# Kernel tuning notes

Hardware: AMD Instinct MI355X
Metric: run time of the kernel (lower is better)

Reference implementation:

```python
import jax, jax.numpy as jnp
import numpy as np

EMBED_DIM = 1024
NUM_HEADS = 16
HEAD_DIM = EMBED_DIM // NUM_HEADS
STD = 0.02


def setup_inputs() -> dict:
    key = jax.random.key(0)
    k1, k2, k3 = jax.random.split(key, 3)
    B, S = 2, 2048
    inputs = jax.random.normal(k1, (B, S, EMBED_DIM), dtype=jnp.float32)
    # qkv projection: Linear(E, 3E); torch Linear weight is [out, in]
    w_qkv = jax.random.normal(k2, (3 * EMBED_DIM, EMBED_DIM), dtype=jnp.float32) * STD
    b_qkv = jnp.zeros((3 * EMBED_DIM,), dtype=jnp.float32)
    w_out = jax.random.normal(k3, (EMBED_DIM, EMBED_DIM), dtype=jnp.float32) * STD
    b_out = jnp.zeros((EMBED_DIM,), dtype=jnp.float32)
    return {"inputs": inputs, "w_qkv": w_qkv, "b_qkv": b_qkv, "w_out": w_out, "b_out": b_out}


def reference(inputs, w_qkv, b_qkv, w_out, b_out):
    B, S, E = inputs.shape
    qkv = inputs @ w_qkv.T + b_qkv                      # [B,S,3E]
    q, k, v = jnp.split(qkv, 3, axis=2)                 # each [B,S,E]

    def split_heads(t):
        return t.reshape(B, S, NUM_HEADS, HEAD_DIM).transpose(0, 2, 1, 3)  # [B,H,S,D]

    q, k, v = split_heads(q), split_heads(k), split_heads(v)
    scores = jnp.einsum('bhqd,bhkd->bhqk', q, k) * (1.0 / np.sqrt(HEAD_DIM))
    causal = jnp.tril(jnp.ones((S, S), dtype=bool))     # [S,S]
    scores = jnp.where(causal[None, None, :, :], scores, -jnp.inf)
    probs = jax.nn.softmax(scores, axis=-1)             # dropout is identity in eval mode
    ctx = jnp.einsum('bhqk,bhkd->bhqd', probs, v)       # [B,H,S,D]
    ctx = ctx.transpose(0, 2, 1, 3).reshape(B, S, E)
    return ctx @ w_out.T + b_out
```

## Files before the change

### kernel.cpp

```cpp
#include <hip/hip_runtime.h>
#include <hip/hip_bf16.h>

#define BATCH 2
#define SEQ   2048
#define EMB   1024
#define NHEAD 16
#define HDIM  64
#define MTOT  (BATCH*SEQ)
#define KTOT  EMB

#define NX  (MTOT*EMB)
#define NW1 (3*EMB*EMB)
#define NW2 (EMB*EMB)
#define NCVT (NX+NW1+NW2)

typedef short bf8 __attribute__((ext_vector_type(8)));
typedef short s4v __attribute__((ext_vector_type(4)));
typedef float f4  __attribute__((ext_vector_type(4)));
typedef unsigned int uint;

__device__ __forceinline__ short f2b(float f) {
    __hip_bfloat16 h = __float2bfloat16(f);
    return __builtin_bit_cast(short, h);
}
__device__ __forceinline__ void gl_lds16(const short* g, short* l) {
    __builtin_amdgcn_global_load_lds(
        (const __attribute__((address_space(1))) uint*)g,
        (__attribute__((address_space(3))) uint*)l, 16, 0, 0);
}
#define SWZ_SRC(lane)      ((((lane) ^ ((lane)>>2) ^ ((lane)>>4)) & 3) * 8)
#define SWZ_RD(quad, l16)  ((((quad) ^ (l16) ^ ((l16)>>2)) & 3) * 8)

__global__ __launch_bounds__(256) void cvt_all(
    const float* __restrict__ X, const float* __restrict__ W1,
    const float* __restrict__ W2,
    short* __restrict__ xb, short* __restrict__ w1b, short* __restrict__ w2b)
{
    int i4 = (blockIdx.x * 256 + threadIdx.x) * 4;
    const float* src; short* dst; int off;
    if (i4 < NX)            { src = X;  dst = xb;  off = i4; }
    else if (i4 < NX + NW1) { src = W1; dst = w1b; off = i4 - NX; }
    else                    { src = W2; dst = w2b; off = i4 - NX - NW1; }
    float4 v = *(const float4*)&src[off];
    s4v o; o[0]=f2b(v.x); o[1]=f2b(v.y); o[2]=f2b(v.z); o[3]=f2b(v.w);
    *(s4v*)&dst[off] = o;
}

__global__ __launch_bounds__(256) void gemm_qkv(
    const short* __restrict__ Xb, const short* __restrict__ Wb,
    const float* __restrict__ bias,
    short* __restrict__ qb, short* __restrict__ kb, short* __restrict__ vtb)
{
    __shared__ __align__(16) short As[2*128*32];
    __shared__ __align__(16) short Bs[2*128*32];
    const int tid  = threadIdx.x;
    const int lane = tid & 63;
    const int w    = tid >> 6;
    const int l16  = lane & 15, quad = lane >> 4;
    const int wm   = (w >> 1) * 64, wn = (w & 1) * 64;
    const int srow = (lane >> 2);
    const int scol = SWZ_SRC(lane);

    const int id  = blockIdx.x;
    const int xcd = id & 7, k = id >> 3;
    const int rg  = k / 12, p = k - rg*12;
    const int R   = rg*8 + xcd;
    const int bm  = (R & 7)*4 + (p & 3);
    const int bn  = (R >> 3)*3 + (p >> 2);

    f4 acc[4][4] = {};
    for (int k0 = 0; k0 < KTOT; k0 += 64) {
        #pragma unroll
        for (int t = 0; t < 4; t++) {
            const int rr = w*32 + (t & 1)*16;
            const int kc = t >> 1;
            int ra = bm*128 + rr + srow;
            gl_lds16(&Xb[(size_t)ra*KTOT + k0 + kc*32 + scol], &As[kc*4096 + rr*32]);
            int rb = bn*128 + rr + srow;
            gl_lds16(&Wb[(size_t)rb*KTOT + k0 + kc*32 + scol], &Bs[kc*4096 + rr*32]);
        }
        __syncthreads();
        #pragma unroll
        for (int kc = 0; kc < 2; kc++) {
            bf8 af[4], bf[4];
            #pragma unroll
            for (int t = 0; t < 4; t++) {
                af[t] = *(const bf8*)&As[kc*4096 + (wm + t*16 + l16)*32 + SWZ_RD(quad, l16)];
                bf[t] = *(const bf8*)&Bs[kc*4096 + (wn + t*16 + l16)*32 + SWZ_RD(quad, l16)];
            }
            #pragma unroll
            for (int mt = 0; mt < 4; mt++)
                #pragma unroll
                for (int nt = 0; nt < 4; nt++)
                    acc[mt][nt] = __builtin_amdgcn_mfma_f32_16x16x32_bf16(af[mt], bf[nt], acc[mt][nt], 0, 0, 0);
        }
        __syncthreads();
    }
    #pragma unroll
    for (int mt = 0; mt < 4; mt++)
    #pragma unroll
    for (int nt = 0; nt < 4; nt++) {
        int colg = bn*128 + wn + nt*16 + l16;
        float bv = bias[colg];
        #pragma unroll
        for (int r = 0; r < 4; r++) {
            int rowg = bm*128 + wm + mt*16 + quad*4 + r;
            short h = f2b(acc[mt][nt][r] + bv);
            int bb = rowg >> 11, s = rowg & 2047;
            if (colg < 1024) {
                int hh = colg >> 6, d = colg & 63;
                qb[(((bb*NHEAD + hh)*SEQ + s) << 6) + d] = h;
            } else if (colg < 2048) {
                int c2 = colg - 1024, hh = c2 >> 6, d = c2 & 63;
                kb[(((bb*NHEAD + hh)*SEQ + s) << 6) + d] = h;
            } else {
                int c3 = colg - 2048, hh = c3 >> 6, d = c3 & 63;
                int ssw = (s & ~63) | (((s & 15) << 2) | ((s >> 4) & 3));
                vtb[((bb*NHEAD + hh)*HDIM + d)*SEQ + ssw] = h;
            }
        }
    }
}

__global__ __launch_bounds__(256, 3) void attn(
    const short* __restrict__ qb, const short* __restrict__ kb,
    const short* __restrict__ vtb, short* __restrict__ ctx)
{
    __shared__ __align__(16) short Ks[2*4096];
    __shared__ __align__(16) short Vs[2*4096];
    __shared__ __align__(16) short pl[4][32*64];
    const int tid = threadIdx.x;
    const int w = tid >> 6, lane = tid & 63;
    const int l16 = lane & 15, quad = lane >> 4;
    const int f  = blockIdx.x;
    const int xcd = f & 7, j = f >> 3;
    const int bh  = xcd*4 + (j & 3);
    const int slot = j >> 2;
    const int s3 = slot & 7;
    const int hq = slot >> 3;
    const int tq = hq ? (15 - s3) : s3;
    const int q0w = tq*128 + w*16;
    const int base = bh * (SEQ*HDIM);
    short* myp = pl[w];
    const float SC = 0.125f * 1.44269504f;

    const int lq  = lane >> 2;
    const int lsw = SWZ_SRC(lane);

    const bool isk = (w < 2);
    short* tb = isk ? Ks : Vs;
    const int sstep = isk ? 64*HDIM : 64;
    const short* sp0; const short* sp1; const short* sp2; const short* sp3;
    int dof[4];
    {
        const int wb2 = (w & 1) * 4;
        #pragma unroll
        for (int tt = 0; tt < 4; tt++) {
            int t = wb2 + tt, cc = t & 1, g = (t >> 1) & 3;
            dof[tt] = (cc*64 + g*16)*32;
            const short* s = isk ? &kb[base + (g*16 + lq)*HDIM + cc*32 + lsw]
                                 : &vtb[base + (g*16 + lq)*SEQ + cc*32 + lsw];
            if (tt == 0) sp0 = s; else if (tt == 1) sp1 = s;
            else if (tt == 2) sp2 = s; else sp3 = s;
        }
    }

    bf8 qa[2][2];
    #pragma unroll
    for (int rg = 0; rg < 2; rg++)
        #pragma unroll
        for (int kc = 0; kc < 2; kc++)
            qa[rg][kc] = *(const bf8*)&qb[base + (q0w + rg*64 + l16)*HDIM + kc*32 + quad*8];

    f4 oA[4] = {}, oB[4] = {};
    float lacc[2][4] = {};
    const int rdK = l16*32 + SWZ_RD(quad, l16);
    const int nst = 2*tq + 2;

    gl_lds16(sp0, tb + dof[0]); gl_lds16(sp1, tb + dof[1]);
    gl_lds16(sp2, tb + dof[2]); gl_lds16(sp3, tb + dof[3]);
    sp0 += sstep; sp1 += sstep; sp2 += sstep; sp3 += sstep;
    __syncthreads();

    int buf = 0;
    for (int st = 0; st < nst; st++) {
        if (st < nst - 1) {
            short* d = tb + (buf ^ 1)*4096;
            gl_lds16(sp0, d + dof[0]); gl_lds16(sp1, d + dof[1]);
            gl_lds16(sp2, d + dof[2]); gl_lds16(sp3, d + dof[3]);
            sp0 += sstep; sp1 += sstep; sp2 += sstep; sp3 += sstep;
        }
        const int kbase = buf*4096 + rdK;
        const bool rg0act = (st <= 2*tq);
        #pragma unroll
        for (int rg = 0; rg < 2; rg++) {
            if (rg == 0 && !rg0act) continue;
            f4 s[4] = {};
            #pragma unroll
            for (int kf = 0; kf < 4; kf++)
                #pragma unroll
                for (int c = 0; c < 2; c++) {
                    bf8 kfr = *(const bf8*)&Ks[kbase + (c*64 + kf*16)*32];
                    s[kf] = __builtin_amdgcn_mfma_f32_16x16x32_bf16(qa[rg][c], kfr, s[kf], 0, 0, 0);
                }
            const bool diag = (st == 2*tq + rg);
            if (diag) {
                const int j0 = st*64;
                #pragma unroll
                for (int r = 0; r < 4; r++) {
                    const int row = quad*4 + r;
                    const int qi  = q0w + rg*64 + row;
                    float e[4];
                    #pragma unroll
                    for (int kf = 0; kf < 4; kf++) {
                        e[kf] = __builtin_amdgcn_exp2f(s[kf][r] * SC);
                        if (j0 + kf*16 + l16 > qi) e[kf] = 0.0f;
                        lacc[rg][r] += e[kf];
                    }
                    uint u01 = __builtin_amdgcn_perm(__builtin_bit_cast(uint, e[1]),
                                                     __builtin_bit_cast(uint, e[0]), 0x07060302u);
                    uint u23 = __builtin_amdgcn_perm(__builtin_bit_cast(uint, e[3]),
                                                     __builtin_bit_cast(uint, e[2]), 0x07060302u);
                    uint2 pk = {u01, u23};
                    int c8 = ((l16 >> 1) ^ (row & 7));
                    *(uint2*)&myp[(rg*16 + row)*64 + c8*8 + (l16 & 1)*4] = pk;
                }
            } else {
                #pragma unroll
                for (int r = 0; r < 4; r++) {
                    const int row = quad*4 + r;
                    float e[4];
                    #pragma unroll
                    for (int kf = 0; kf < 4; kf++) {
                        e[kf] = __builtin_amdgcn_exp2f(s[kf][r] * SC);
                        lacc[rg][r] += e[kf];
                    }
                    uint u01 = __builtin_amdgcn_perm(__builtin_bit_cast(uint, e[1]),
                                                     __builtin_bit_cast(uint, e[0]), 0x07060302u);
                    uint u23 = __builtin_amdgcn_perm(__builtin_bit_cast(uint, e[3]),
                                                     __builtin_bit_cast(uint, e[2]), 0x07060302u);
                    uint2 pk = {u01, u23};
                    int c8 = ((l16 >> 1) ^ (row & 7));
                    *(uint2*)&myp[(rg*16 + row)*64 + c8*8 + (l16 & 1)*4] = pk;
                }
            }
        }
        asm volatile("" ::: "memory");
        if (rg0act) {
            bf8 pa[2];
            #pragma unroll
            for (int kc = 0; kc < 2; kc++)
                pa[kc] = *(const bf8*)&myp[l16*64 + (((kc*4 + quad) ^ (l16 & 7)))*8];
            #pragma unroll
            for (int dt = 0; dt < 4; dt++)
                #pragma unroll
                for (int c = 0; c < 2; c++) {
                    bf8 vf = *(const bf8*)&Vs[kbase + (c*64 + dt*16)*32];
                    oA[dt] = __builtin_amdgcn_mfma_f32_16x16x32_bf16(pa[c], vf, oA[dt], 0, 0, 0);
                }
        }
        {
            bf8 pa[2];
            #pragma unroll
            for (int kc = 0; kc < 2; kc++)
                pa[kc] = *(const bf8*)&myp[(16 + l16)*64 + (((kc*4 + quad) ^ (l16 & 7)))*8];
            #pragma unroll
            for (int dt = 0; dt < 4; dt++)
                #pragma unroll
                for (int c = 0; c < 2; c++) {
                    bf8 vf = *(const bf8*)&Vs[kbase + (c*64 + dt*16)*32];
                    oB[dt] = __builtin_amdgcn_mfma_f32_16x16x32_bf16(pa[c], vf, oB[dt], 0, 0, 0);
                }
        }
        __syncthreads();
        buf ^= 1;
    }
    #pragma unroll
    for (int rg = 0; rg < 2; rg++)
        #pragma unroll
        for (int r = 0; r < 4; r++) {
            float v = lacc[rg][r];
            v += __shfl_xor(v, 1);
            v += __shfl_xor(v, 2);
            v += __shfl_xor(v, 4);
            v += __shfl_xor(v, 8);
            lacc[rg][r] = v;
        }
    const int b = bh >> 4, h = bh & 15;
    #pragma unroll
    for (int rg = 0; rg < 2; rg++)
        #pragma unroll
        for (int r = 0; r < 4; r++) {
            float inv = 1.0f / lacc[rg][r];
            int qi = q0w + rg*64 + quad*4 + r;
            int rowoff = (b*SEQ + qi)*EMB + h*HDIM;
            #pragma unroll
            for (int dt = 0; dt < 4; dt++)
                ctx[rowoff + dt*16 + l16] = f2b((rg ? oB[dt][r] : oA[dt][r]) * inv);
        }
}

__global__ __launch_bounds__(256) void gemm_out(
    const short* __restrict__ A, const short* __restrict__ Wb,
    const float* __restrict__ bias, float* __restrict__ out)
{
    __shared__ __align__(16) short As[2*128*32];
    __shared__ __align__(16) short Bs[2*64*32];
    const int f = blockIdx.x;
    const int xcd = f & 7, j = f >> 3;
    const int bm  = (xcd & 3)*8 + (j & 7);
    const int bn  = (xcd >> 2)*8 + (j >> 3);
    const int tid  = threadIdx.x;
    const int lane = tid & 63;
    const int w    = tid >> 6;
    const int l16  = lane & 15, quad = lane >> 4;
    const int wm   = (w >> 1) * 64, wn = (w & 1) * 32;
    const int srow = (lane >> 2);
    const int scol = SWZ_SRC(lane);
    f4 acc[4][2] = {};
    for (int k0 = 0; k0 < KTOT; k0 += 64) {
        #pragma unroll
        for (int t = 0; t < 4; t++) {
            const int a  = w*4 + t;
            const int kc = a & 1, g = a >> 1;
            int ra = bm*128 + g*16 + srow;
            gl_lds16(&A[(size_t)ra*KTOT + k0 + kc*32 + scol], &As[kc*4096 + g*16*32]);
        }
        #pragma unroll
        for (int t = 0; t < 2; t++) {
            const int b  = w*2 + t;
            const int kc = b & 1, g = b >> 1;
            int rb = bn*64 + g*16 + srow;
            gl_lds16(&Wb[(size_t)rb*KTOT + k0 + kc*32 + scol], &Bs[kc*2048 + g*16*32]);
        }
        __syncthreads();
        #pragma unroll
        for (int kc = 0; kc < 2; kc++) {
            bf8 af[4], bf[2];
            #pragma unroll
            for (int t = 0; t < 4; t++)
                af[t] = *(const bf8*)&As[kc*4096 + (wm + t*16 + l16)*32 + SWZ_RD(quad, l16)];
            #pragma unroll
            for (int t = 0; t < 2; t++)
                bf[t] = *(const bf8*)&Bs[kc*2048 + (wn + t*16 + l16)*32 + SWZ_RD(quad, l16)];
            #pragma unroll
            for (int mt = 0; mt < 4; mt++)
                #pragma unroll
                for (int nt = 0; nt < 2; nt++)
                    acc[mt][nt] = __builtin_amdgcn_mfma_f32_16x16x32_bf16(af[mt], bf[nt], acc[mt][nt], 0, 0, 0);
        }
        __syncthreads();
    }
    #pragma unroll
    for (int mt = 0; mt < 4; mt++)
    #pragma unroll
    for (int nt = 0; nt < 2; nt++) {
        int colg = bn*64 + wn + nt*16 + l16;
        float bv = bias[colg];
        #pragma unroll
        for (int r = 0; r < 4; r++) {
            int rowg = bm*128 + wm + mt*16 + quad*4 + r;
            out[(size_t)rowg*EMB + colg] = acc[mt][nt][r] + bv;
        }
    }
}

extern "C" void kernel_launch(void* const* d_in, const int* in_sizes, int n_in,
                              void* d_out, int out_size, void* d_ws, size_t ws_size,
                              hipStream_t stream) {
    const float* X    = (const float*)d_in[0];
    const float* Wqkv = (const float*)d_in[1];
    const float* Bqkv = (const float*)d_in[2];
    const float* Wout = (const float*)d_in[3];
    const float* Bout = (const float*)d_in[4];
    float* out = (float*)d_out;

    short* xb    = (short*)d_ws;
    short* w1b   = xb  + NX;
    short* w2b   = w1b + NW1;
    short* qb    = w2b + NW2;
    short* kb    = qb  + NX;
    short* vtb   = kb  + NX;
    short* ctx   = vtb + NX;

    cvt_all<<<NCVT/1024, 256, 0, stream>>>(X, Wqkv, Wout, xb, w1b, w2b);
    gemm_qkv<<<dim3(768), 256, 0, stream>>>(xb, w1b, Bqkv, qb, kb, vtb);
    attn<<<dim3(512), 256, 0, stream>>>(qb, kb, vtb, ctx);
    gemm_out<<<dim3(512), 256, 0, stream>>>(ctx, w2b, Bout, out);
}
```

Measured before the change: 175.0 us.

## Double-buffer LDS tiles in QKV GEMM to overlap global loads with MFMA

The QKV projection GEMM now uses two LDS buffers per operand and issues the direct-to-LDS loads for the next K slice before computing on the current one. Global pointer arithmetic is hoisted out of the loop. The aim is to hide global-memory latency behind MFMA work. LDS use doubles to 64KB per block, which may reduce occupancy. The hunk does not show whether the loop tail still syncs correctly before a buffer is reused.

```diff
diff --git a/kernel.cpp b/kernel.cpp
--- a/kernel.cpp
+++ b/kernel.cpp
@@ -51,8 +51,8 @@
     const float* __restrict__ bias,
     short* __restrict__ qb, short* __restrict__ kb, short* __restrict__ vtb)
 {
-    __shared__ __align__(16) short As[2*128*32];
-    __shared__ __align__(16) short Bs[2*128*32];
+    __shared__ __align__(16) short As[2*2*128*32];
+    __shared__ __align__(16) short Bs[2*2*128*32];
     const int tid  = threadIdx.x;
     const int lane = tid & 63;
     const int w    = tid >> 6;
@@ -68,25 +68,41 @@
     const int bm  = (R & 7)*4 + (p & 3);
     const int bn  = (R >> 3)*3 + (p >> 2);
 
+    const short* pa[4]; const short* pb[4]; int dd[4];
+    #pragma unroll
+    for (int t = 0; t < 4; t++) {
+        const int rr = w*32 + (t & 1)*16;
+        const int kc = t >> 1;
+        pa[t] = &Xb[(size_t)(bm*128 + rr + srow)*KTOT + kc*32 + scol];
+        pb[t] = &Wb[(size_t)(bn*128 + rr + srow)*KTOT + kc*32 + scol];
+        dd[t] = kc*4096 + rr*32;
+    }
+
     f4 acc[4][4] = {};
-    for (int k0 = 0; k0 < KTOT; k0 += 64) {
-        #pragma unroll
-        for (int t = 0; t < 4; t++) {
-            const int rr = w*32 + (t & 1)*16;
-            const int kc = t >> 1;
-            int ra = bm*128 + rr + srow;
-            gl_lds16(&Xb[(size_t)ra*KTOT + k0 + kc*32 + scol], &As[kc*4096 + rr*32]);
-            int rb = bn*128 + rr + srow;
-            gl_lds16(&Wb[(size_t)rb*KTOT + k0 + kc*32 + scol], &Bs[kc*4096 + rr*32]);
-        }
-        __syncthreads();
+
+    #pragma unroll
+    for (int t = 0; t < 4; t++) { gl_lds16(pa[t], &As[dd[t]]); gl_lds16(pb[t], &Bs[dd[t]]); }
+    __syncthreads();
+
+    for (int t = 0; t < 16; t++) {
+        const int buf = t & 1;
+        if (t < 15) {
+            const int bo = (buf ^ 1) * 8192;
+            const int ko = (t + 1) * 64;
+            #pragma unroll
+            for (int s = 0; s < 4; s++) {
+                gl_lds16(pa[s] + ko, &As[bo + dd[s]]);
+                gl_lds16(pb[s] + ko, &Bs[bo + dd[s]]);
+            }
+        }
+        const int ab = buf * 8192;
         #pragma unroll
         for (int kc = 0; kc < 2; kc++) {
             bf8 af[4], bf[4];
             #pragma unroll
-            for (int t = 0; t < 4; t++) {
-                af[t] = *(const bf8*)&As[kc*4096 + (wm + t*16 + l16)*32 + SWZ_RD(quad, l16)];
-                bf[t] = *(const bf8*)&Bs[kc*4096 + (wn + t*16 + l16)*32 + SWZ_RD(quad, l16)];
+            for (int s = 0; s < 4; s++) {
+                af[s] = *(const bf8*)&As[ab + kc*4096 + (wm + s*16 + l16)*32 + SWZ_RD(quad, l16)];
+                bf[s] = *(const bf8*)&Bs[ab + kc*4096 + (wn + s*16 + l16)*32 + SWZ_RD(quad, l16)];
             }
             #pragma unroll
             for (int mt = 0; mt < 4; mt++)
```

Measured after the change: 194.0 us. 1.11x slower.

## Double-buffer QKV GEMM LDS tiles to overlap global loads with MFMA

Applied to the files above, without the earlier changes.

Restructures the QKV projection GEMM main loop into 32-wide k steps over two LDS buffers. The loads for the next step are issued into the alternate buffer before the MFMAs on the current one, instead of load, barrier, compute, barrier. Row base addresses are hoisted out of the loop. This aims to hide global-to-LDS latency behind compute, at the cost of a barrier per 32-wide step and a smaller compute chunk between barriers.

```diff
diff --git a/kernel.cpp b/kernel.cpp
--- a/kernel.cpp
+++ b/kernel.cpp
@@ -68,32 +68,43 @@
     const int bm  = (R & 7)*4 + (p & 3);
     const int bn  = (R >> 3)*3 + (p >> 2);
 
+    const size_t arow0 = (size_t)(bm*128 + w*32 +  0 + srow)*KTOT + scol;
+    const size_t arow1 = (size_t)(bm*128 + w*32 + 16 + srow)*KTOT + scol;
+    const size_t brow0 = (size_t)(bn*128 + w*32 +  0 + srow)*KTOT + scol;
+    const size_t brow1 = (size_t)(bn*128 + w*32 + 16 + srow)*KTOT + scol;
+    const int d0 = (w*32 +  0)*32;
+    const int d1 = (w*32 + 16)*32;
+
     f4 acc[4][4] = {};
-    for (int k0 = 0; k0 < KTOT; k0 += 64) {
+
+    gl_lds16(&Xb[arow0], &As[d0]); gl_lds16(&Xb[arow1], &As[d1]);
+    gl_lds16(&Wb[brow0], &Bs[d0]); gl_lds16(&Wb[brow1], &Bs[d1]);
+    __syncthreads();
+
+    #pragma unroll 2
+    for (int h = 0; h < 32; h++) {
+        const int reg = h & 1;
+        if (h < 31) {
+            const int hn  = h + 1;
+            const int off = (hn >> 1)*64 + (hn & 1)*32;
+            const int dr  = (hn & 1)*4096;
+            gl_lds16(&Xb[arow0 + off], &As[dr + d0]);
+            gl_lds16(&Xb[arow1 + off], &As[dr + d1]);
+            gl_lds16(&Wb[brow0 + off], &Bs[dr + d0]);
+            gl_lds16(&Wb[brow1 + off], &Bs[dr + d1]);
+        }
+        asm volatile("" ::: "memory");
+        bf8 af[4], bf[4];
         #pragma unroll
         for (int t = 0; t < 4; t++) {
-            const int rr = w*32 + (t & 1)*16;
-            const int kc = t >> 1;
-            int ra = bm*128 + rr + srow;
-            gl_lds16(&Xb[(size_t)ra*KTOT + k0 + kc*32 + scol], &As[kc*4096 + rr*32]);
-            int rb = bn*128 + rr + srow;
-            gl_lds16(&Wb[(size_t)rb*KTOT + k0 + kc*32 + scol], &Bs[kc*4096 + rr*32]);
-        }
-        __syncthreads();
-        #pragma unroll
-        for (int kc = 0; kc < 2; kc++) {
-            bf8 af[4], bf[4];
-            #pragma unroll
-            for (int t = 0; t < 4; t++) {
-                af[t] = *(const bf8*)&As[kc*4096 + (wm + t*16 + l16)*32 + SWZ_RD(quad, l16)];
-                bf[t] = *(const bf8*)&Bs[kc*4096 + (wn + t*16 + l16)*32 + SWZ_RD(quad, l16)];
-            }
-            #pragma unroll
-            for (int mt = 0; mt < 4; mt++)
-                #pragma unroll
-                for (int nt = 0; nt < 4; nt++)
-                    acc[mt][nt] = __builtin_amdgcn_mfma_f32_16x16x32_bf16(af[mt], bf[nt], acc[mt][nt], 0, 0, 0);
-        }
+            af[t] = *(const bf8*)&As[reg*4096 + (wm + t*16 + l16)*32 + SWZ_RD(quad, l16)];
+            bf[t] = *(const bf8*)&Bs[reg*4096 + (wn + t*16 + l16)*32 + SWZ_RD(quad, l16)];
+        }
+        #pragma unroll
+        for (int mt = 0; mt < 4; mt++)
+            #pragma unroll
+            for (int nt = 0; nt < 4; nt++)
+                acc[mt][nt] = __builtin_amdgcn_mfma_f32_16x16x32_bf16(af[mt], bf[nt], acc[mt][nt], 0, 0, 0);
         __syncthreads();
     }
     #pragma unroll
```

Result: no change. 173.3 us (median of 3 runs) (-1.0%).
